# Performance work log

Hardware: AMD Instinct MI355X
Metric: run time of the kernel (lower is better)

Reference implementation:

```python
import jax, jax.numpy as jnp
import numpy as np

D_IN = 32
K = 16


def cbr(x, W, s, b):
    # 1x1 Conv2d + folded (eval-mode) BatchNorm + ReLU, channels-last.
    return jax.nn.relu(jnp.einsum('...i,io->...o', x, W) * s + b)


def gather_neighbour(pc, idx):
    # pc: [B, N, d]; idx: [B, N, K] -> [B, N, K, d]
    B, N, d = pc.shape
    g = jnp.take_along_axis(pc, idx.reshape(B, -1, 1), axis=1)
    return g.reshape(B, N, K, d)


def setup_inputs() -> dict:
    key = jax.random.key(0)
    ks = jax.random.split(key, 32)
    B, N = 2, 65536

    def w(k, ci, co):
        return jax.random.normal(k, (ci, co), jnp.float32) * (1.0 / np.sqrt(ci))

    inp = {
        'feature': jax.random.normal(ks[0], (B, D_IN, N, 1), jnp.float32),
        'xyz': jax.random.normal(ks[1], (B, N, 3), jnp.float32),
        'neigh_idx': jax.random.randint(ks[2], (B, N, K), 0, N, jnp.int64),
        # TNet
        'tW1': w(ks[3], 3, 16),  'ts1': jnp.ones(16),  'tb1': jnp.zeros(16),
        'tW2': w(ks[4], 16, 64), 'ts2': jnp.ones(64),  'tb2': jnp.zeros(64),
        'tW3': w(ks[5], 64, 16), 'ts3': jnp.ones(16),  'tb3': jnp.zeros(16),
        'tW4': w(ks[6], 16, 9),  'tb4': jnp.zeros(9),
        # RFA mlps
        'W1': w(ks[7], 3, 3),            's1': jnp.ones(3),     'b1': jnp.zeros(3),
        'W2': w(ks[8], D_IN, D_IN),      's2': jnp.ones(D_IN),  'b2': jnp.zeros(D_IN),
        'W3': w(ks[9], D_IN + 3, D_IN),  's3': jnp.ones(D_IN),  'b3': jnp.zeros(D_IN),
        'W4': w(ks[10], 2 * D_IN, D_IN), 's4': jnp.ones(D_IN),  'b4': jnp.zeros(D_IN),
    }
    return inp


def tnet(xyz, tW1, ts1, tb1, tW2, ts2, tb2, tW3, ts3, tb3, tW4, tb4):
    h = cbr(xyz, tW1, ts1, tb1)          # [B, N, 16]
    h = cbr(h, tW2, ts2, tb2)            # [B, N, 64]
    h = jnp.max(h, axis=1, keepdims=True)  # [B, 1, 64]
    h = cbr(h, tW3, ts3, tb3)            # [B, 1, 16]
    h = jnp.einsum('...i,io->...o', h, tW4) + tb4  # [B, 1, 9] (no bn/act)
    dia = jnp.eye(3, dtype=h.dtype).reshape(1, 1, 9)
    return (h + dia).reshape(-1, 3, 3)


def reference(feature, xyz, neigh_idx,
              tW1, ts1, tb1, tW2, ts2, tb2, tW3, ts3, tb3, tW4, tb4,
              W1, s1, b1, W2, s2, b2, W3, s3, b3, W4, s4, b4):
    # channels-last features [B, N, d_in]
    feat = feature.squeeze(-1).transpose(0, 2, 1)

    t = tnet(xyz, tW1, ts1, tb1, tW2, ts2, tb2, tW3, ts3, tb3, tW4, tb4)
    f_xyz = jnp.einsum('bni,bij->bnj', xyz, t)   # [B, N, 3]
    f_xyz = cbr(f_xyz, W1, s1, b1)               # [B, N, 3]
    f_xyz = gather_neighbour(f_xyz, neigh_idx)   # [B, N, K, 3]

    f_nei = cbr(feat, W2, s2, b2)                # [B, N, d]
    f_nei = gather_neighbour(f_nei, neigh_idx)   # [B, N, K, d]

    f_cat = jnp.concatenate([f_nei, f_xyz], axis=-1)  # [B, N, K, d+3]
    f_cat = cbr(f_cat, W3, s3, b3)               # [B, N, K, d]
    f_cat = jnp.max(f_cat, axis=2)               # max pooling over K -> [B, N, d]

    f = jnp.concatenate([feat, f_cat], axis=-1)  # [B, N, 2d]
    f = cbr(f, W4, s4, b4)                       # [B, N, d_in]
    return f.transpose(0, 2, 1)[..., None]       # [B, d_in, N, 1]
```

## Files before the change

### kernel.cpp

```cpp
#include <hip/hip_runtime.h>

#define NPTS   65536
#define TOTAL  (2 * NPTS)
#define NUNITS 1024

typedef __attribute__((ext_vector_type(8)))  short short8;
typedef __attribute__((ext_vector_type(16))) float float16;
union F8 { uint4 u; short8 s; };

#define WS_STRIPE 0
#define WS_T1A    8192
#define WS_T1B    (8192 + TOTAL * 64)
#define WS_T2     (8192 + TOTAL * 64 + TOTAL * 8)

__device__ __forceinline__ unsigned short f2bf(float x) {
    unsigned u = __float_as_uint(x);
    return (unsigned short)((u + 0x7FFFu + ((u >> 16) & 1u)) >> 16);
}
__device__ __forceinline__ unsigned pk2(float a, float b) {
    return (unsigned)f2bf(a) | ((unsigned)f2bf(b) << 16);
}
__device__ __forceinline__ float relu(float x) { return x > 0.f ? x : 0.f; }
__device__ __forceinline__ uint4 pk8(const float* e) {
    uint4 u;
    u.x = pk2(e[0], e[1]); u.y = pk2(e[2], e[3]);
    u.z = pk2(e[4], e[5]); u.w = pk2(e[6], e[7]);
    return u;
}
__device__ __forceinline__ float16 zero16() {
    float16 z;
#pragma unroll
    for (int i = 0; i < 16; i++) z[i] = 0.f;
    return z;
}

__global__ __launch_bounds__(256) void kP0(
    const float* __restrict__ feature, const float* __restrict__ xyz,
    const float* __restrict__ tW1, const float* __restrict__ ts1, const float* __restrict__ tb1,
    const float* __restrict__ tW2, const float* __restrict__ ts2, const float* __restrict__ tb2,
    const float* __restrict__ W2,  const float* __restrict__ s2,  const float* __restrict__ b2,
    char* ws)
{
    __shared__ float red[4][64];
    float* stripe       = (float*)(ws + WS_STRIPE);
    unsigned short* t1a = (unsigned short*)(ws + WS_T1A);
    unsigned short* t2  = (unsigned short*)(ws + WS_T2);
    const int lane = threadIdx.x & 63, wv = threadIdx.x >> 6;
    const int col = lane & 31, h = lane >> 5;
    const float16 z = zero16();
    const int u = blockIdx.x;
    const int b = u >> 9;
    float e[8];
    float aw0[8], aw1[8], aw2[8], bb[8];
#pragma unroll
    for (int j = 0; j < 8; j++) {
        int k = 8 * h + j; float s = ts1[k];
        aw0[j] = tW1[k] * s; aw1[j] = tW1[16 + k] * s; aw2[j] = tW1[32 + k] * s;
        bb[j] = tb1[k];
    }
    F8 bf0, bf1;
#pragma unroll
    for (int j = 0; j < 8; j++) e[j] = tW2[(8 * h + j) * 64 + col] * ts2[col];
    bf0.u = pk8(e);
#pragma unroll
    for (int j = 0; j < 8; j++) e[j] = tW2[(8 * h + j) * 64 + 32 + col] * ts2[32 + col];
    bf1.u = pk8(e);
    F8 a0, a1;
    float sc2 = s2[col];
#pragma unroll
    for (int j = 0; j < 8; j++) e[j] = W2[(8 * h + j) * 32 + col] * sc2;
    a0.u = pk8(e);
#pragma unroll
    for (int j = 0; j < 8; j++) e[j] = W2[(16 + 8 * h + j) * 32 + col] * sc2;
    a1.u = pk8(e);
    float b2v[16];
#pragma unroll
    for (int r = 0; r < 16; r++) b2v[r] = b2[(r & 3) + 8 * (r >> 2) + 4 * h];

    int base = u * 128 + wv * 32;
    const float* xp = xyz + (size_t)(base + col) * 3;
    float x0 = xp[0], x1 = xp[1], x2 = xp[2];
    float hv[8];
#pragma unroll
    for (int j = 0; j < 8; j++)
        hv[j] = relu(x0 * aw0[j] + x1 * aw1[j] + x2 * aw2[j] + bb[j]);
    F8 af; af.u = pk8(hv);
    float16 c0 = __builtin_amdgcn_mfma_f32_32x32x16_bf16(af.s, bf0.s, z, 0, 0, 0);
    float16 c1 = __builtin_amdgcn_mfma_f32_32x32x16_bf16(af.s, bf1.s, z, 0, 0, 0);
    float v0 = c0[0], v1 = c1[0];
#pragma unroll
    for (int i = 1; i < 16; i++) { v0 = fmaxf(v0, c0[i]); v1 = fmaxf(v1, c1[i]); }
    v0 = fmaxf(v0, __shfl_xor(v0, 32));
    v1 = fmaxf(v1, __shfl_xor(v1, 32));
    if (h == 0) { red[wv][col] = v0; red[wv][32 + col] = v1; }
    __syncthreads();
    if (threadIdx.x < 64) {
        int c = threadIdx.x;
        float m = fmaxf(fmaxf(red[0][c], red[1][c]), fmaxf(red[2][c], red[3][c]));
        float val = relu(m + tb2[c]);
        atomicMax((unsigned*)(stripe + (u & 15) * 128 + b * 64 + c), __float_as_uint(val));
    }
    int pt = base + col;
    const float* fb = feature + (size_t)b * 32 * NPTS + (pt & (NPTS - 1));
    float v[8];
    F8 f0, f1;
#pragma unroll
    for (int j = 0; j < 8; j++) v[j] = fb[(size_t)(8 * h + j) * NPTS];
    f0.u = pk8(v);
#pragma unroll
    for (int j = 0; j < 8; j++) v[j] = fb[(size_t)(16 + 8 * h + j) * NPTS];
    f1.u = pk8(v);
    *(uint4*)(t2 + (size_t)pt * 32 + 8 * h) = f0.u;
    *(uint4*)(t2 + (size_t)pt * 32 + 16 + 8 * h) = f1.u;
    float16 acc = z;
    acc = __builtin_amdgcn_mfma_f32_32x32x16_bf16(a0.s, f0.s, acc, 0, 0, 0);
    acc = __builtin_amdgcn_mfma_f32_32x32x16_bf16(a1.s, f1.s, acc, 0, 0, 0);
#pragma unroll
    for (int q = 0; q < 4; q++) {
        int r = 4 * q;
        uint2 uu;
        uu.x = pk2(relu(acc[r] + b2v[r]), relu(acc[r + 1] + b2v[r + 1]));
        uu.y = pk2(relu(acc[r + 2] + b2v[r + 2]), relu(acc[r + 3] + b2v[r + 3]));
        *(uint2*)(t1a + (size_t)pt * 32 + 8 * q + 4 * h) = uu;
    }
}

__global__ __launch_bounds__(256) void kP1(
    const float* __restrict__ xyz,
    const float* __restrict__ tW3, const float* __restrict__ ts3, const float* __restrict__ tb3,
    const float* __restrict__ tW4, const float* __restrict__ tb4,
    const float* __restrict__ W1,  const float* __restrict__ s1, const float* __restrict__ b1,
    char* ws)
{
    const float* stripe = (const float*)(ws + WS_STRIPE);
    unsigned short* t1b = (unsigned short*)(ws + WS_T1B);
    const int lane = threadIdx.x & 63, wv = threadIdx.x >> 6;
    const int col = lane & 31, h = lane >> 5;
    const int u = blockIdx.x;
    const int b = u >> 9;
    float hm = 0.f;
#pragma unroll
    for (int s = 0; s < 16; s++)
        hm = fmaxf(hm, stripe[s * 128 + b * 64 + lane]);
    float v[16];
    const float4* trow = (const float4*)(tW3 + lane * 16);
#pragma unroll
    for (int q = 0; q < 4; q++) {
        float4 t4 = trow[q];
        v[4 * q + 0] = hm * t4.x; v[4 * q + 1] = hm * t4.y;
        v[4 * q + 2] = hm * t4.z; v[4 * q + 3] = hm * t4.w;
    }
#pragma unroll
    for (int off = 1; off < 64; off <<= 1) {
#pragma unroll
        for (int c = 0; c < 16; c++) v[c] += __shfl_xor(v[c], off);
    }
    float T[9];
#pragma unroll
    for (int j = 0; j < 9; j++) T[j] = tb4[j];
#pragma unroll
    for (int c = 0; c < 16; c++) {
        float h3 = relu(v[c] * ts3[c] + tb3[c]);
#pragma unroll
        for (int j = 0; j < 9; j++) T[j] += h3 * tW4[c * 9 + j];
    }
    T[0] += 1.f; T[4] += 1.f; T[8] += 1.f;

    int pt = u * 128 + wv * 32 + col;
    const float* xp = xyz + (size_t)pt * 3;
    float x0 = xp[0], x1 = xp[1], x2 = xp[2];
    float q0 = x0 * T[0] + x1 * T[3] + x2 * T[6];
    float q1 = x0 * T[1] + x1 * T[4] + x2 * T[7];
    float q2 = x0 * T[2] + x1 * T[5] + x2 * T[8];
    float r0 = relu((q0 * W1[0] + q1 * W1[3] + q2 * W1[6]) * s1[0] + b1[0]);
    float r1 = relu((q0 * W1[1] + q1 * W1[4] + q2 * W1[7]) * s1[1] + b1[1]);
    float r2 = relu((q0 * W1[2] + q1 * W1[5] + q2 * W1[8]) * s1[2] + b1[2]);
    if (h == 0) {
        uint2 uu; uu.x = pk2(r0, r1); uu.y = pk2(r2, 0.f);
        *(uint2*)(t1b + (size_t)pt * 4) = uu;
    }
}

__global__ __launch_bounds__(256) void kP23(
    const int* __restrict__ nidx,
    const float* __restrict__ W3, const float* __restrict__ s3, const float* __restrict__ b3,
    const float* __restrict__ W4, const float* __restrict__ s4, const float* __restrict__ b4,
    char* ws, float* __restrict__ out)
{
    __shared__ unsigned short mld[128 * 36];
    const unsigned short* t1a = (const unsigned short*)(ws + WS_T1A);
    const unsigned short* t1b = (const unsigned short*)(ws + WS_T1B);
    const unsigned short* t2  = (const unsigned short*)(ws + WS_T2);
    const int lane = threadIdx.x & 63, wv = threadIdx.x >> 6;
    const int col = lane & 31, h = lane >> 5;
    const float16 z = zero16();
    float e[8];
    F8 w0, w1, w2, zf;
    zf.u.x = zf.u.y = zf.u.z = zf.u.w = 0u;
    float sc3 = s3[col];
#pragma unroll
    for (int j = 0; j < 8; j++) e[j] = W3[(8 * h + j) * 32 + col] * sc3;
    w0.u = pk8(e);
#pragma unroll
    for (int j = 0; j < 8; j++) e[j] = W3[(16 + 8 * h + j) * 32 + col] * sc3;
    w1.u = pk8(e);
    w2 = zf;
    if (h == 0) {
        float e2[8] = {0.f, 0.f, 0.f, 0.f, 0.f, 0.f, 0.f, 0.f};
#pragma unroll
        for (int j = 0; j < 3; j++) e2[j] = W3[(32 + j) * 32 + col] * sc3;
        w2.u = pk8(e2);
    }
    float b3v = b3[col];
    F8 aw[4];
    float sc4 = s4[col];
#pragma unroll
    for (int t = 0; t < 4; t++) {
#pragma unroll
        for (int j = 0; j < 8; j++) e[j] = W4[(16 * t + 8 * h + j) * 32 + col] * sc4;
        aw[t].u = pk8(e);
    }
    float b4v[16];
#pragma unroll
    for (int r = 0; r < 16; r++) b4v[r] = b4[(r & 3) + 8 * (r >> 2) + 4 * h];

    int slot = blockIdx.x & 7, batch = slot >> 2;
    int grp = (blockIdx.x >> 3) * 4 + (slot & 3);
    int u = batch * 512 + grp;
    int base = u * 128;

    int idxs[16];
#pragma unroll
    for (int it = 0; it < 16; it++)
        idxs[it] = nidx[(base + 2 * (wv * 16 + it)) * 16 + col];

    F8 na0, na1, na2;
    {
        size_t row = ((size_t)batch << 16) + (unsigned)idxs[0];
        const unsigned short* ap = t1a + row * 32;
        na0.u = *(const uint4*)(ap + 8 * h);
        na1.u = *(const uint4*)(ap + 16 + 8 * h);
        na2 = zf;
        if (h == 0) { uint2 q = *(const uint2*)(t1b + row * 4); na2.u.x = q.x; na2.u.y = q.y; }
    }
    for (int it = 0; it < 16; it++) {
        F8 ca0 = na0, ca1 = na1, ca2 = na2;
        if (it < 15) {
            size_t row = ((size_t)batch << 16) + (unsigned)idxs[it + 1];
            const unsigned short* ap = t1a + row * 32;
            na0.u = *(const uint4*)(ap + 8 * h);
            na1.u = *(const uint4*)(ap + 16 + 8 * h);
            na2 = zf;
            if (h == 0) { uint2 q = *(const uint2*)(t1b + row * 4); na2.u.x = q.x; na2.u.y = q.y; }
        }
        float16 acc = z;
        acc = __builtin_amdgcn_mfma_f32_32x32x16_bf16(ca0.s, w0.s, acc, 0, 0, 0);
        acc = __builtin_amdgcn_mfma_f32_32x32x16_bf16(ca1.s, w1.s, acc, 0, 0, 0);
        acc = __builtin_amdgcn_mfma_f32_32x32x16_bf16(ca2.s, w2.s, acc, 0, 0, 0);
        float vA = acc[0], vB = acc[8];
#pragma unroll
        for (int r = 1; r < 8; r++) { vA = fmaxf(vA, acc[r]); vB = fmaxf(vB, acc[8 + r]); }
        vA = fmaxf(vA, __shfl_xor(vA, 32));
        vB = fmaxf(vB, __shfl_xor(vB, 32));
        vA = relu(vA + b3v);
        vB = relu(vB + b3v);
        float val = h ? vB : vA;
        int pi = wv * 16 + it;
        mld[(2 * pi + h) * 36 + col] = f2bf(val);
    }

    int p_loc = wv * 32 + col;
    int p = base + p_loc;
    const unsigned short* bp = t2 + (size_t)p * 32 + 8 * h;
    F8 x0, x1, x2, x3;
    x0.u = *(const uint4*)(bp);
    x1.u = *(const uint4*)(bp + 16);
    const unsigned short* mp = mld + p_loc * 36;
    uint2 q0 = *(const uint2*)(mp + 8 * h);
    uint2 q1 = *(const uint2*)(mp + 8 * h + 4);
    uint2 q2 = *(const uint2*)(mp + 16 + 8 * h);
    uint2 q3 = *(const uint2*)(mp + 16 + 8 * h + 4);
    x2.u.x = q0.x; x2.u.y = q0.y; x2.u.z = q1.x; x2.u.w = q1.y;
    x3.u.x = q2.x; x3.u.y = q2.y; x3.u.z = q3.x; x3.u.w = q3.y;
    float16 acc = z;
    acc = __builtin_amdgcn_mfma_f32_32x32x16_bf16(aw[0].s, x0.s, acc, 0, 0, 0);
    acc = __builtin_amdgcn_mfma_f32_32x32x16_bf16(aw[1].s, x1.s, acc, 0, 0, 0);
    acc = __builtin_amdgcn_mfma_f32_32x32x16_bf16(aw[2].s, x2.s, acc, 0, 0, 0);
    acc = __builtin_amdgcn_mfma_f32_32x32x16_bf16(aw[3].s, x3.s, acc, 0, 0, 0);
    float* ob = out + (size_t)(batch * 32) * NPTS + (p & (NPTS - 1));
#pragma unroll
    for (int r = 0; r < 16; r++) {
        int o = (r & 3) + 8 * (r >> 2) + 4 * h;
        ob[(size_t)o * NPTS] = relu(acc[r] + b4v[r]);
    }
}

extern "C" void kernel_launch(void* const* d_in, const int* in_sizes, int n_in,
                              void* d_out, int out_size, void* d_ws, size_t ws_size,
                              hipStream_t stream)
{
    const float* feature = (const float*)d_in[0];
    const float* xyz     = (const float*)d_in[1];
    const int*   nidx    = (const int*)d_in[2];
    const float* tW1 = (const float*)d_in[3];
    const float* ts1 = (const float*)d_in[4];
    const float* tb1 = (const float*)d_in[5];
    const float* tW2 = (const float*)d_in[6];
    const float* ts2 = (const float*)d_in[7];
    const float* tb2 = (const float*)d_in[8];
    const float* tW3 = (const float*)d_in[9];
    const float* ts3 = (const float*)d_in[10];
    const float* tb3 = (const float*)d_in[11];
    const float* tW4 = (const float*)d_in[12];
    const float* tb4 = (const float*)d_in[13];
    const float* W1  = (const float*)d_in[14];
    const float* s1  = (const float*)d_in[15];
    const float* b1  = (const float*)d_in[16];
    const float* W2  = (const float*)d_in[17];
    const float* s2  = (const float*)d_in[18];
    const float* b2  = (const float*)d_in[19];
    const float* W3  = (const float*)d_in[20];
    const float* s3  = (const float*)d_in[21];
    const float* b3  = (const float*)d_in[22];
    const float* W4  = (const float*)d_in[23];
    const float* s4  = (const float*)d_in[24];
    const float* b4  = (const float*)d_in[25];
    (void)in_sizes; (void)n_in; (void)out_size; (void)ws_size;

    char* wsp = (char*)d_ws;
    float* outp = (float*)d_out;

    hipMemsetAsync(wsp + WS_STRIPE, 0, 16 * 128 * sizeof(float), stream);
    kP0<<<NUNITS, 256, 0, stream>>>(feature, xyz, tW1, ts1, tb1, tW2, ts2, tb2,
                                    W2, s2, b2, wsp);
    kP1<<<NUNITS, 256, 0, stream>>>(xyz, tW3, ts3, tb3, tW4, tb4, W1, s1, b1, wsp);
    kP23<<<NUNITS, 256, 0, stream>>>(nidx, W3, s3, b3, W4, s4, b4, wsp, outp);
}
```

Before: 160.7 us.

## Fuse TNet finalize and xyz MLP into gather kernel, drop intermediate buffers

```diff
diff --git a/kernel.cpp b/kernel.cpp
--- a/kernel.cpp
+++ b/kernel.cpp
@@ -9,9 +9,7 @@
 union F8 { uint4 u; short8 s; };
 
 #define WS_STRIPE 0
-#define WS_T1A    8192
-#define WS_T1B    (8192 + TOTAL * 64)
-#define WS_T2     (8192 + TOTAL * 64 + TOTAL * 8)
+#define WS_T1A    262144
 
 __device__ __forceinline__ unsigned short f2bf(float x) {
     unsigned u = __float_as_uint(x);
@@ -34,7 +32,7 @@
     return z;
 }
 
-__global__ __launch_bounds__(256) void kP0(
+__global__ __launch_bounds__(256) void kA(
     const float* __restrict__ feature, const float* __restrict__ xyz,
     const float* __restrict__ tW1, const float* __restrict__ ts1, const float* __restrict__ tb1,
     const float* __restrict__ tW2, const float* __restrict__ ts2, const float* __restrict__ tb2,
@@ -44,7 +42,6 @@
     __shared__ float red[4][64];
     float* stripe       = (float*)(ws + WS_STRIPE);
     unsigned short* t1a = (unsigned short*)(ws + WS_T1A);
-    unsigned short* t2  = (unsigned short*)(ws + WS_T2);
     const int lane = threadIdx.x & 63, wv = threadIdx.x >> 6;
     const int col = lane & 31, h = lane >> 5;
     const float16 z = zero16();
@@ -97,8 +94,7 @@
     if (threadIdx.x < 64) {
         int c = threadIdx.x;
         float m = fmaxf(fmaxf(red[0][c], red[1][c]), fmaxf(red[2][c], red[3][c]));
-        float val = relu(m + tb2[c]);
-        atomicMax((unsigned*)(stripe + (u & 15) * 128 + b * 64 + c), __float_as_uint(val));
+        stripe[u * 64 + c] = relu(m + tb2[c]);
     }
     int pt = base + col;
     const float* fb = feature + (size_t)b * 32 * NPTS + (pt & (NPTS - 1));
@@ -110,8 +106,6 @@
 #pragma unroll
     for (int j = 0; j < 8; j++) v[j] = fb[(size_t)(16 + 8 * h + j) * NPTS];
     f1.u = pk8(v);
-    *(uint4*)(t2 + (size_t)pt * 32 + 8 * h) = f0.u;
-    *(uint4*)(t2 + (size_t)pt * 32 + 16 + 8 * h) = f1.u;
     float16 acc = z;
     acc = __builtin_amdgcn_mfma_f32_32x32x16_bf16(a0.s, f0.s, acc, 0, 0, 0);
     acc = __builtin_amdgcn_mfma_f32_32x32x16_bf16(a1.s, f1.s, acc, 0, 0, 0);
@@ -125,75 +119,72 @@
     }
 }
 
-__global__ __launch_bounds__(256) void kP1(
-    const float* __restrict__ xyz,
+__global__ __launch_bounds__(256) void kB(
+    const float* __restrict__ feature, const float* __restrict__ xyz,
+    const int* __restrict__ nidx,
     const float* __restrict__ tW3, const float* __restrict__ ts3, const float* __restrict__ tb3,
     const float* __restrict__ tW4, const float* __restrict__ tb4,
     const float* __restrict__ W1,  const float* __restrict__ s1, const float* __restrict__ b1,
-    char* ws)
-{
-    const float* stripe = (const float*)(ws + WS_STRIPE);
-    unsigned short* t1b = (unsigned short*)(ws + WS_T1B);
-    const int lane = threadIdx.x & 63, wv = threadIdx.x >> 6;
-    const int col = lane & 31, h = lane >> 5;
-    const int u = blockIdx.x;
-    const int b = u >> 9;
-    float hm = 0.f;
-#pragma unroll
-    for (int s = 0; s < 16; s++)
-        hm = fmaxf(hm, stripe[s * 128 + b * 64 + lane]);
-    float v[16];
-    const float4* trow = (const float4*)(tW3 + lane * 16);
-#pragma unroll
-    for (int q = 0; q < 4; q++) {
-        float4 t4 = trow[q];
-        v[4 * q + 0] = hm * t4.x; v[4 * q + 1] = hm * t4.y;
-        v[4 * q + 2] = hm * t4.z; v[4 * q + 3] = hm * t4.w;
-    }
-#pragma unroll
-    for (int off = 1; off < 64; off <<= 1) {
-#pragma unroll
-        for (int c = 0; c < 16; c++) v[c] += __shfl_xor(v[c], off);
-    }
-    float T[9];
-#pragma unroll
-    for (int j = 0; j < 9; j++) T[j] = tb4[j];
-#pragma unroll
-    for (int c = 0; c < 16; c++) {
-        float h3 = relu(v[c] * ts3[c] + tb3[c]);
-#pragma unroll
-        for (int j = 0; j < 9; j++) T[j] += h3 * tW4[c * 9 + j];
-    }
-    T[0] += 1.f; T[4] += 1.f; T[8] += 1.f;
-
-    int pt = u * 128 + wv * 32 + col;
-    const float* xp = xyz + (size_t)pt * 3;
-    float x0 = xp[0], x1 = xp[1], x2 = xp[2];
-    float q0 = x0 * T[0] + x1 * T[3] + x2 * T[6];
-    float q1 = x0 * T[1] + x1 * T[4] + x2 * T[7];
-    float q2 = x0 * T[2] + x1 * T[5] + x2 * T[8];
-    float r0 = relu((q0 * W1[0] + q1 * W1[3] + q2 * W1[6]) * s1[0] + b1[0]);
-    float r1 = relu((q0 * W1[1] + q1 * W1[4] + q2 * W1[7]) * s1[1] + b1[1]);
-    float r2 = relu((q0 * W1[2] + q1 * W1[5] + q2 * W1[8]) * s1[2] + b1[2]);
-    if (h == 0) {
-        uint2 uu; uu.x = pk2(r0, r1); uu.y = pk2(r2, 0.f);
-        *(uint2*)(t1b + (size_t)pt * 4) = uu;
-    }
-}
-
-__global__ __launch_bounds__(256) void kP23(
-    const int* __restrict__ nidx,
-    const float* __restrict__ W3, const float* __restrict__ s3, const float* __restrict__ b3,
-    const float* __restrict__ W4, const float* __restrict__ s4, const float* __restrict__ b4,
+    const float* __restrict__ W3,  const float* __restrict__ s3, const float* __restrict__ b3,
+    const float* __restrict__ W4,  const float* __restrict__ s4, const float* __restrict__ b4,
     char* ws, float* __restrict__ out)
 {
+    __shared__ float redh[4][64];
+    __shared__ float Tsh[9];
     __shared__ unsigned short mld[128 * 36];
+    const float* stripe       = (const float*)(ws + WS_STRIPE);
     const unsigned short* t1a = (const unsigned short*)(ws + WS_T1A);
-    const unsigned short* t1b = (const unsigned short*)(ws + WS_T1B);
-    const unsigned short* t2  = (const unsigned short*)(ws + WS_T2);
     const int lane = threadIdx.x & 63, wv = threadIdx.x >> 6;
     const int col = lane & 31, h = lane >> 5;
     const float16 z = zero16();
+
+    int slot = blockIdx.x & 7, batch = slot >> 2;
+    int grp = (blockIdx.x >> 3) * 4 + (slot & 3);
+    int base = (batch * 512 + grp) * 128;
+
+    int idxs[16];
+#pragma unroll
+    for (int it = 0; it < 16; it++)
+        idxs[it] = nidx[(base + 2 * (wv * 16 + it)) * 16 + col];
+
+    {
+        int c = threadIdx.x & 63, part = threadIdx.x >> 6;
+        const float* sp = stripe + (size_t)(batch * 512 + part * 128) * 64 + c;
+        float hm = 0.f;
+#pragma unroll 8
+        for (int s = 0; s < 128; s++) hm = fmaxf(hm, sp[s * 64]);
+        redh[part][c] = hm;
+    }
+    __syncthreads();
+    if (wv == 0) {
+        float hm = fmaxf(fmaxf(redh[0][lane], redh[1][lane]),
+                         fmaxf(redh[2][lane], redh[3][lane]));
+        float v[16];
+        const float4* trow = (const float4*)(tW3 + lane * 16);
+#pragma unroll
+        for (int q = 0; q < 4; q++) {
+            float4 t4 = trow[q];
+            v[4 * q + 0] = hm * t4.x; v[4 * q + 1] = hm * t4.y;
+            v[4 * q + 2] = hm * t4.z; v[4 * q + 3] = hm * t4.w;
+        }
+#pragma unroll
+        for (int off = 1; off < 64; off <<= 1) {
+#pragma unroll
+            for (int c = 0; c < 16; c++) v[c] += __shfl_xor(v[c], off);
+        }
+        float T[9];
+#pragma unroll
+        for (int j = 0; j < 9; j++) T[j] = tb4[j];
+#pragma unroll
+        for (int c = 0; c < 16; c++) {
+            float h3 = relu(v[c] * ts3[c] + tb3[c]);
+#pragma unroll
+            for (int j = 0; j < 9; j++) T[j] += h3 * tW4[c * 9 + j];
+        }
+        T[0] += 1.f; T[4] += 1.f; T[8] += 1.f;
+        if (lane < 9) Tsh[lane] = T[lane];
+    }
+
     float e[8];
     F8 w0, w1, w2, zf;
     zf.u.x = zf.u.y = zf.u.z = zf.u.w = 0u;
@@ -223,75 +214,102 @@
     float b4v[16];
 #pragma unroll
     for (int r = 0; r < 16; r++) b4v[r] = b4[(r & 3) + 8 * (r >> 2) + 4 * h];
-
-    int slot = blockIdx.x & 7, batch = slot >> 2;
-    int grp = (blockIdx.x >> 3) * 4 + (slot & 3);
-    int u = batch * 512 + grp;
-    int base = u * 128;
-
-    int idxs[16];
-#pragma unroll
-    for (int it = 0; it < 16; it++)
-        idxs[it] = nidx[(base + 2 * (wv * 16 + it)) * 16 + col];
-
-    F8 na0, na1, na2;
+    float W1f[9], b1v[3];
+#pragma unroll
+    for (int j = 0; j < 9; j++) W1f[j] = W1[j] * s1[j % 3];
+#pragma unroll
+    for (int j = 0; j < 3; j++) b1v[j] = b1[j];
+
+    int p_loc = wv * 32 + col;
+    int p = base + p_loc;
     {
-        size_t row = ((size_t)batch << 16) + (unsigned)idxs[0];
-        const unsigned short* ap = t1a + row * 32;
-        na0.u = *(const uint4*)(ap + 8 * h);
-        na1.u = *(const uint4*)(ap + 16 + 8 * h);
-        na2 = zf;
-        if (h == 0) { uint2 q = *(const uint2*)(t1b + row * 4); na2.u.x = q.x; na2.u.y = q.y; }
-    }
-    for (int it = 0; it < 16; it++) {
-        F8 ca0 = na0, ca1 = na1, ca2 = na2;
-        if (it < 15) {
-            size_t row = ((size_t)batch << 16) + (unsigned)idxs[it + 1];
+        const float* fb = feature + (size_t)batch * 32 * NPTS + (p & (NPTS - 1));
+        float v[8];
+#pragma unroll
+        for (int j = 0; j < 8; j++) v[j] = fb[(size_t)(8 * h + j) * NPTS];
+        e[0] = v[0];
+        F8 xf0, xf1;
+        xf0.u = pk8(v);
+#pragma unroll
+        for (int j = 0; j < 8; j++) v[j] = fb[(size_t)(16 + 8 * h + j) * NPTS];
+        xf1.u = pk8(v);
+        w2 = w2;
+        __syncthreads();
+
+        float T[9];
+#pragma unroll
+        for (int j = 0; j < 9; j++) T[j] = Tsh[j];
+
+        F8 na0, na1;
+        float nx0 = 0.f, nx1 = 0.f, nx2 = 0.f;
+        {
+            size_t row = ((size_t)batch << 16) + (unsigned)idxs[0];
             const unsigned short* ap = t1a + row * 32;
             na0.u = *(const uint4*)(ap + 8 * h);
             na1.u = *(const uint4*)(ap + 16 + 8 * h);
-            na2 = zf;
-            if (h == 0) { uint2 q = *(const uint2*)(t1b + row * 4); na2.u.x = q.x; na2.u.y = q.y; }
-        }
+            if (h == 0) {
+                const float* nxp = xyz + row * 3;
+                nx0 = nxp[0]; nx1 = nxp[1]; nx2 = nxp[2];
+            }
+        }
+        for (int it = 0; it < 16; it++) {
+            F8 ca0 = na0, ca1 = na1;
+            float cx0 = nx0, cx1 = nx1, cx2 = nx2;
+            if (it < 15) {
+                size_t row = ((size_t)batch << 16) + (unsigned)idxs[it + 1];
+                const unsigned short* ap = t1a + row * 32;
+                na0.u = *(const uint4*)(ap + 8 * h);
+                na1.u = *(const uint4*)(ap + 16 + 8 * h);
+                if (h == 0) {
+                    const float* nxp = xyz + row * 3;
+                    nx0 = nxp[0]; nx1 = nxp[1]; nx2 = nxp[2];
+                }
+            }
+            F8 ca2 = zf;
+            if (h == 0) {
+                float q0 = cx0 * T[0] + cx1 * T[3] + cx2 * T[6];
+                float q1 = cx0 * T[1] + cx1 * T[4] + cx2 * T[7];
+                float q2 = cx0 * T[2] + cx1 * T[5] + cx2 * T[8];
+                float r0 = relu(q0 * W1f[0] + q1 * W1f[3] + q2 * W1f[6] + b1v[0]);
+                float r1 = relu(q0 * W1f[1] + q1 * W1f[4] + q2 * W1f[7] + b1v[1]);
+                float r2 = relu(q0 * W1f[2] + q1 * W1f[5] + q2 * W1f[8] + b1v[2]);
+                ca2.u.x = pk2(r0, r1); ca2.u.y = pk2(r2, 0.f);
+            }
+            float16 acc = z;
+            acc = __builtin_amdgcn_mfma_f32_32x32x16_bf16(ca0.s, w0.s, acc, 0, 0, 0);
+            acc = __builtin_amdgcn_mfma_f32_32x32x16_bf16(ca1.s, w1.s, acc, 0, 0, 0);
+            acc = __builtin_amdgcn_mfma_f32_32x32x16_bf16(ca2.s, w2.s, acc, 0, 0, 0);
+            float vA = acc[0], vB = acc[8];
+#pragma unroll
+            for (int r = 1; r < 8; r++) { vA = fmaxf(vA, acc[r]); vB = fmaxf(vB, acc[8 + r]); }
+            vA = fmaxf(vA, __shfl_xor(vA, 32));
+            vB = fmaxf(vB, __shfl_xor(vB, 32));
+            vA = relu(vA + b3v);
+            vB = relu(vB + b3v);
+            float val = h ? vB : vA;
+            int pi = wv * 16 + it;
+            mld[(2 * pi + h) * 36 + col] = f2bf(val);
+        }
+
+        const unsigned short* mp = mld + p_loc * 36;
+        uint2 q0 = *(const uint2*)(mp + 8 * h);
+        uint2 q1 = *(const uint2*)(mp + 8 * h + 4);
+        uint2 q2 = *(const uint2*)(mp + 16 + 8 * h);
+        uint2 q3 = *(const uint2*)(mp + 16 + 8 * h + 4);
+        F8 xm0, xm1;
+        xm0.u.x = q0.x; xm0.u.y = q0.y; xm0.u.z = q1.x; xm0.u.w = q1.y;
+        xm1.u.x = q2.x; xm1.u.y = q2.y; xm1.u.z = q3.x; xm1.u.w = q3.y;
         float16 acc = z;
-        acc = __builtin_amdgcn_mfma_f32_32x32x16_bf16(ca0.s, w0.s, acc, 0, 0, 0);
-        acc = __builtin_amdgcn_mfma_f32_32x32x16_bf16(ca1.s, w1.s, acc, 0, 0, 0);
-        acc = __builtin_amdgcn_mfma_f32_32x32x16_bf16(ca2.s, w2.s, acc, 0, 0, 0);
-        float vA = acc[0], vB = acc[8];
-#pragma unroll
-        for (int r = 1; r < 8; r++) { vA = fmaxf(vA, acc[r]); vB = fmaxf(vB, acc[8 + r]); }
-        vA = fmaxf(vA, __shfl_xor(vA, 32));
-        vB = fmaxf(vB, __shfl_xor(vB, 32));
-        vA = relu(vA + b3v);
-        vB = relu(vB + b3v);
-        float val = h ? vB : vA;
-        int pi = wv * 16 + it;
-        mld[(2 * pi + h) * 36 + col] = f2bf(val);
-    }
-
-    int p_loc = wv * 32 + col;
-    int p = base + p_loc;
-    const unsigned short* bp = t2 + (size_t)p * 32 + 8 * h;
-    F8 x0, x1, x2, x3;
-    x0.u = *(const uint4*)(bp);
-    x1.u = *(const uint4*)(bp + 16);
-    const unsigned short* mp = mld + p_loc * 36;
-    uint2 q0 = *(const uint2*)(mp + 8 * h);
-    uint2 q1 = *(const uint2*)(mp + 8 * h + 4);
-    uint2 q2 = *(const uint2*)(mp + 16 + 8 * h);
-    uint2 q3 = *(const uint2*)(mp + 16 + 8 * h + 4);
-    x2.u.x = q0.x; x2.u.y = q0.y; x2.u.z = q1.x; x2.u.w = q1.y;
-    x3.u.x = q2.x; x3.u.y = q2.y; x3.u.z = q3.x; x3.u.w = q3.y;
-    float16 acc = z;
-    acc = __builtin_amdgcn_mfma_f32_32x32x16_bf16(aw[0].s, x0.s, acc, 0, 0, 0);
-    acc = __builtin_amdgcn_mfma_f32_32x32x16_bf16(aw[1].s, x1.s, acc, 0, 0, 0);
-    acc = __builtin_amdgcn_mfma_f32_32x32x16_bf16(aw[2].s, x2.s, acc, 0, 0, 0);
-    acc = __builtin_amdgcn_mfma_f32_32x32x16_bf16(aw[3].s, x3.s, acc, 0, 0, 0);
-    float* ob = out + (size_t)(batch * 32) * NPTS + (p & (NPTS - 1));
-#pragma unroll
-    for (int r = 0; r < 16; r++) {
-        int o = (r & 3) + 8 * (r >> 2) + 4 * h;
-        ob[(size_t)o * NPTS] = relu(acc[r] + b4v[r]);
+        acc = __builtin_amdgcn_mfma_f32_32x32x16_bf16(aw[0].s, xf0.s, acc, 0, 0, 0);
+        acc = __builtin_amdgcn_mfma_f32_32x32x16_bf16(aw[1].s, xf1.s, acc, 0, 0, 0);
+        acc = __builtin_amdgcn_mfma_f32_32x32x16_bf16(aw[2].s, xm0.s, acc, 0, 0, 0);
+        acc = __builtin_amdgcn_mfma_f32_32x32x16_bf16(aw[3].s, xm1.s, acc, 0, 0, 0);
+        float* ob = out + (size_t)(batch * 32) * NPTS + (p & (NPTS - 1));
+#pragma unroll
+        for (int r = 0; r < 16; r++) {
+            int o = (r & 3) + 8 * (r >> 2) + 4 * h;
+            ob[(size_t)o * NPTS] = relu(acc[r] + b4v[r]);
+        }
     }
 }
 
@@ -330,9 +348,8 @@
     char* wsp = (char*)d_ws;
     float* outp = (float*)d_out;
 
-    hipMemsetAsync(wsp + WS_STRIPE, 0, 16 * 128 * sizeof(float), stream);
-    kP0<<<NUNITS, 256, 0, stream>>>(feature, xyz, tW1, ts1, tb1, tW2, ts2, tb2,
-                                    W2, s2, b2, wsp);
-    kP1<<<NUNITS, 256, 0, stream>>>(xyz, tW3, ts3, tb3, tW4, tb4, W1, s1, b1, wsp);
-    kP23<<<NUNITS, 256, 0, stream>>>(nidx, W3, s3, b3, W4, s4, b4, wsp, outp);
-}
+    kA<<<NUNITS, 256, 0, stream>>>(feature, xyz, tW1, ts1, tb1, tW2, ts2, tb2,
+                                   W2, s2, b2, wsp);
+    kB<<<NUNITS, 256, 0, stream>>>(feature, xyz, nidx, tW3, ts3, tb3, tW4, tb4,
+                                   W1, s1, b1, W3, s3, b3, W4, s4, b4, wsp, outp);
+}
```

New measurement: 198.0 us. 1.23x slower.
